# Kernel optimization log

Measured on AMD Instinct MI355X. Metric: run time of the kernel, lower is better.

## Reference

```python
import jax, jax.numpy as jnp
import numpy as np

B, N, K, IN_C, OUT_C = 8, 20000, 9, 64, 64


def setup_inputs() -> dict:
    key = jax.random.key(0)
    k1, k2, k3, k4, k5, k6 = jax.random.split(key, 6)
    x = jax.random.normal(k1, (B, N, IN_C), dtype=jnp.float32)
    neighbor_index = jax.random.randint(k2, (B, N, K), 0, N, dtype=jnp.int64)
    # adjweight initialized to identity per original code (eye expanded over num_pts)
    adjweight = jnp.broadcast_to(jnp.eye(K, dtype=jnp.float32), (N, K, K))
    # conv: Linear(in_c*K -> out_c); mlp_out: Linear(in_c -> out_c)
    conv_w = jax.random.normal(k3, (OUT_C, IN_C * K), dtype=jnp.float32) / np.sqrt(IN_C * K)
    conv_b = jax.random.normal(k4, (OUT_C,), dtype=jnp.float32) * 0.01
    mlp_w = jax.random.normal(k5, (OUT_C, IN_C), dtype=jnp.float32) / np.sqrt(IN_C)
    mlp_b = jax.random.normal(k6, (OUT_C,), dtype=jnp.float32) * 0.01
    return {"x": x, "neighbor_index": neighbor_index, "adjweight": adjweight,
            "conv_w": conv_w, "conv_b": conv_b, "mlp_w": mlp_w, "mlp_b": mlp_b}


def reference(x, neighbor_index, adjweight, conv_w, conv_b, mlp_w, mlp_b):
    bsize, num_pts, feats = x.shape
    num_neighbor = neighbor_index.shape[-1]
    # zero_padding mask: last point zeroed
    mask = jnp.ones((1, num_pts, 1), dtype=x.dtype).at[0, -1, 0].set(0.0)
    x = x * mask
    # per-batch gather of neighbor features: [B, N, K, F]
    x_neighbors = jax.vmap(lambda xb, ib: xb[ib])(x, neighbor_index)
    # learnable per-point KxK mixing over the neighbor dim: bnkf,nkt->bntf
    x_neighbors = jnp.einsum('bnkf,nkt->bntf', x_neighbors, adjweight)
    x_neighbors = jax.nn.elu(x_neighbors).reshape(bsize, num_pts, num_neighbor * feats)
    out_feat = jax.nn.elu(x_neighbors @ conv_w.T + conv_b) * mask
    x_res = x @ mlp_w.T + mlp_b
    return out_feat + x_res
```

## Files before the change

### kernel.cpp

```cpp
#include <hip/hip_runtime.h>

#define BB 8
#define NN 20000
#define KK 9
#define KC 576
#define ROWS (BB*NN)

#define WST_ELE   36864
#define WST2_ELE  4096
#define ADJ_ELE   (NN*88)
#define XB_ELE    (ROWS*64)
#define WST_OFF   0
#define WST2_OFF  36864
#define ADJ_OFF   40960
#define XB_OFF    (ADJ_OFF + ADJ_ELE)

typedef __bf16 bf16x8 __attribute__((ext_vector_type(8)));
typedef float  f32x4  __attribute__((ext_vector_type(4)));
typedef unsigned short u16x8 __attribute__((ext_vector_type(8)));
typedef unsigned u32x4 __attribute__((ext_vector_type(4)));

__device__ __forceinline__ unsigned short f2bf(float f) {
    unsigned u = __builtin_bit_cast(unsigned, f);
    u += 0x7FFFu + ((u >> 16) & 1u);
    return (unsigned short)(u >> 16);
}
__device__ __forceinline__ float bfhi2f(unsigned w) { return __builtin_bit_cast(float, w & 0xFFFF0000u); }
__device__ __forceinline__ float bflo2f(unsigned w) { return __builtin_bit_cast(float, w << 16); }
__device__ __forceinline__ float elu_f(float v) { return v > 0.0f ? v : (__expf(v) - 1.0f); }

__global__ void __launch_bounds__(256) paiconv_prep(
        const float* __restrict__ x,
        const float* __restrict__ adj,
        const float* __restrict__ conv_w,
        const float* __restrict__ mlp_w,
        unsigned short* __restrict__ ws16) {
    const int tid = blockIdx.x * 256 + threadIdx.x;

    if (tid < XB_ELE / 8) {
        const int e = tid * 8;
        const int r = e >> 6;
        const int n = r % NN;
        u16x8 pk;
        if (n == NN - 1) {
            #pragma unroll
            for (int i = 0; i < 8; ++i) pk[i] = 0;
        } else {
            f32x4 lo = *(const f32x4*)(x + e);
            f32x4 hi = *(const f32x4*)(x + e + 4);
            #pragma unroll
            for (int i = 0; i < 4; ++i) { pk[i] = f2bf(lo[i]); pk[4 + i] = f2bf(hi[i]); }
        }
        *(u16x8*)(ws16 + XB_OFF + e) = pk;
    }
    if (tid < NN * 11) {
        const int n = tid / 11;
        const int j = (tid - n * 11) * 8;
        u16x8 pk;
        #pragma unroll
        for (int m = 0; m < 8; ++m) {
            const int jj = j + m;
            pk[m] = (jj < 81) ? f2bf(adj[n * 81 + jj]) : (unsigned short)0;
        }
        *(u16x8*)(ws16 + ADJ_OFF + n * 88 + j) = pk;
    }
    if (tid < WST_ELE) {
        const int kk = tid & 31, o = (tid >> 5) & 63, mch = tid >> 11;
        const int c = mch / 9, t = mch - 9 * c;
        ws16[WST_OFF + tid] = f2bf(conv_w[o * KC + t * 64 + c * 32 + kk]);
    }
    if (tid < WST2_ELE) {
        const int kk = tid & 31, o = (tid >> 5) & 63, c2 = tid >> 11;
        ws16[WST2_OFF + tid] = f2bf(mlp_w[o * 64 + c2 * 32 + kk]);
    }
}

__global__ void __launch_bounds__(256, 2) paiconv_main(
        const int*   __restrict__ nidx,
        const float* __restrict__ conv_b,
        const float* __restrict__ mlp_b,
        const unsigned short* __restrict__ ws16,
        float* __restrict__ out) {
    __shared__ float sm[4][16][68];

    const int tx   = threadIdx.x;
    const int lane = tx & 63;
    const int l15  = lane & 15;
    const int q    = lane >> 4;
    const int wave = tx >> 6;
    const int batch = blockIdx.x & 7;
    const int chunk = blockIdx.x >> 3;
    const int n0    = chunk * 64 + wave * 16;
    if (n0 >= NN) return;
    const int rowbase = batch * NN + n0;
    const int myrow   = rowbase + l15;
    const int myn     = n0 + l15;

    const unsigned short* Wst  = ws16 + WST_OFF;
    const unsigned short* Wst2 = ws16 + WST2_OFF;
    const unsigned short* Adj  = ws16 + ADJ_OFF;
    const unsigned short* XB   = ws16 + XB_OFF;
    const unsigned short* XBb  = XB + (size_t)batch * NN * 64;

    int voff[KK];
    #pragma unroll
    for (int k = 0; k < KK; ++k) {
        const int idx = __builtin_nontemporal_load(nidx + myrow * KK + k);
        voff[k] = idx * 64 + q * 8;
    }

    unsigned adjw[44];
    {
        const u32x4* ap = (const u32x4*)(Adj + (size_t)myn * 88);
        #pragma unroll
        for (int u = 0; u < 11; ++u) {
            u32x4 w = __builtin_nontemporal_load(ap + u);
            adjw[4 * u + 0] = w.x; adjw[4 * u + 1] = w.y;
            adjw[4 * u + 2] = w.z; adjw[4 * u + 3] = w.w;
        }
    }

    f32x4 acc[4];
    f32x4 acc2[4];
    #pragma unroll
    for (int ot = 0; ot < 4; ++ot) { acc[ot] = (f32x4)0.0f; acc2[ot] = (f32x4)0.0f; }

    #pragma unroll 1
    for (int c = 0; c < 2; ++c) {
        float v[KK][8];
        #pragma unroll
        for (int k = 0; k < KK; ++k) {
            u16x8 pv = *(const u16x8*)(XBb + voff[k] + c * 32);
            u32x4 pw = __builtin_bit_cast(u32x4, pv);
            v[k][0] = bflo2f(pw.x); v[k][1] = bfhi2f(pw.x);
            v[k][2] = bflo2f(pw.y); v[k][3] = bfhi2f(pw.y);
            v[k][4] = bflo2f(pw.z); v[k][5] = bfhi2f(pw.z);
            v[k][6] = bflo2f(pw.w); v[k][7] = bfhi2f(pw.w);
        }
        #pragma unroll
        for (int t = 0; t < KK; ++t) {
            float m[8] = {0.f,0.f,0.f,0.f,0.f,0.f,0.f,0.f};
            #pragma unroll
            for (int k = 0; k < KK; ++k) {
                const int j = k * 9 + t;
                unsigned w = adjw[j >> 1];
                float a = (j & 1) ? bfhi2f(w) : bflo2f(w);
                #pragma unroll
                for (int i = 0; i < 8; ++i) m[i] = __builtin_fmaf(a, v[k][i], m[i]);
            }
            u16x8 pk;
            #pragma unroll
            for (int i = 0; i < 8; ++i) pk[i] = f2bf(elu_f(m[i]));
            bf16x8 afrag = __builtin_bit_cast(bf16x8, pk);
            const int mch = c * 9 + t;
            #pragma unroll
            for (int ot = 0; ot < 4; ++ot) {
                const u16x8* wp = (const u16x8*)(Wst + mch * 2048 + (ot * 16 + l15) * 32 + q * 8);
                bf16x8 bfrag = __builtin_bit_cast(bf16x8, *wp);
                acc[ot] = __builtin_amdgcn_mfma_f32_16x16x32_bf16(afrag, bfrag, acc[ot], 0, 0, 0);
            }
        }
    }

    #pragma unroll
    for (int c2 = 0; c2 < 2; ++c2) {
        bf16x8 a2 = *(const bf16x8*)(XB + (size_t)myrow * 64 + c2 * 32 + q * 8);
        #pragma unroll
        for (int ot = 0; ot < 4; ++ot) {
            const u16x8* wp = (const u16x8*)(Wst2 + c2 * 2048 + (ot * 16 + l15) * 32 + q * 8);
            bf16x8 b2 = __builtin_bit_cast(bf16x8, *wp);
            acc2[ot] = __builtin_amdgcn_mfma_f32_16x16x32_bf16(a2, b2, acc2[ot], 0, 0, 0);
        }
    }

    #pragma unroll
    for (int ot = 0; ot < 4; ++ot) {
        const int o = ot * 16 + l15;
        const float cb = conv_b[o];
        const float mb = mlp_b[o];
        #pragma unroll
        for (int i = 0; i < 4; ++i) {
            const int rr = 4 * q + i;
            float f = elu_f(acc[ot][i] + cb);
            if (n0 + rr == NN - 1) f = 0.0f;
            f += acc2[ot][i] + mb;
            sm[wave][rr][o] = f;
        }
    }
    #pragma unroll
    for (int p = 0; p < 4; ++p) {
        const int r = p * 4 + q;
        f32x4 vv = *(const f32x4*)&sm[wave][r][l15 * 4];
        __builtin_nontemporal_store(vv, (f32x4*)(out + (size_t)(rowbase + r) * 64 + l15 * 4));
    }
}

extern "C" void kernel_launch(void* const* d_in, const int* in_sizes, int n_in,
                              void* d_out, int out_size, void* d_ws, size_t ws_size,
                              hipStream_t stream) {
    const float* x      = (const float*)d_in[0];
    const int*   nidx   = (const int*)  d_in[1];
    const float* adj    = (const float*)d_in[2];
    const float* conv_w = (const float*)d_in[3];
    const float* conv_b = (const float*)d_in[4];
    const float* mlp_w  = (const float*)d_in[5];
    const float* mlp_b  = (const float*)d_in[6];
    unsigned short* ws16 = (unsigned short*)d_ws;
    float* out = (float*)d_out;

    const int prep_blocks = (XB_ELE / 8) / 256;
    paiconv_prep<<<prep_blocks, 256, 0, stream>>>(x, adj, conv_w, mlp_w, ws16);

    const int main_blocks = 8 * 313;
    paiconv_main<<<main_blocks, 256, 0, stream>>>(nidx, conv_b, mlp_b, ws16, out);
}
```

Baseline: 302.8 us.

## Restructure neighbor gather per-row across lanes and stage mixed features in LDS

The neighbor mixing is reorganised so that each wave processes one point at a time. The lanes span the 64 feature channels, the neighbor indices become wave-uniform scalar loads, and the adjacency weights are read straight from fp32 global memory instead of a bf16 copy made in the prep kernel. The mixed, ELU-activated features are written to an LDS tile, from which the MFMA A-fragments are then loaded. Blocks shrink to 128 threads with twice as many blocks. The intent is to drop the adjacency prep pass and the heavy per-lane register state, in exchange for serialised per-row gather latency, 16 sequential rows per wave, and extra LDS traffic.

```diff
diff --git a/kernel.cpp b/kernel.cpp
--- a/kernel.cpp
+++ b/kernel.cpp
@@ -8,30 +8,29 @@
 
 #define WST_ELE   36864
 #define WST2_ELE  4096
-#define ADJ_ELE   (NN*88)
 #define XB_ELE    (ROWS*64)
 #define WST_OFF   0
 #define WST2_OFF  36864
-#define ADJ_OFF   40960
-#define XB_OFF    (ADJ_OFF + ADJ_ELE)
+#define XB_OFF    40960
+
+#define PSTRIDE 584
 
 typedef __bf16 bf16x8 __attribute__((ext_vector_type(8)));
 typedef float  f32x4  __attribute__((ext_vector_type(4)));
 typedef unsigned short u16x8 __attribute__((ext_vector_type(8)));
-typedef unsigned u32x4 __attribute__((ext_vector_type(4)));
 
 __device__ __forceinline__ unsigned short f2bf(float f) {
     unsigned u = __builtin_bit_cast(unsigned, f);
     u += 0x7FFFu + ((u >> 16) & 1u);
     return (unsigned short)(u >> 16);
 }
-__device__ __forceinline__ float bfhi2f(unsigned w) { return __builtin_bit_cast(float, w & 0xFFFF0000u); }
-__device__ __forceinline__ float bflo2f(unsigned w) { return __builtin_bit_cast(float, w << 16); }
+__device__ __forceinline__ float bf2f(unsigned short h) {
+    return __builtin_bit_cast(float, ((unsigned)h) << 16);
+}
 __device__ __forceinline__ float elu_f(float v) { return v > 0.0f ? v : (__expf(v) - 1.0f); }
 
 __global__ void __launch_bounds__(256) paiconv_prep(
         const float* __restrict__ x,
-        const float* __restrict__ adj,
         const float* __restrict__ conv_w,
         const float* __restrict__ mlp_w,
         unsigned short* __restrict__ ws16) {
@@ -53,17 +52,6 @@
         }
         *(u16x8*)(ws16 + XB_OFF + e) = pk;
     }
-    if (tid < NN * 11) {
-        const int n = tid / 11;
-        const int j = (tid - n * 11) * 8;
-        u16x8 pk;
-        #pragma unroll
-        for (int m = 0; m < 8; ++m) {
-            const int jj = j + m;
-            pk[m] = (jj < 81) ? f2bf(adj[n * 81 + jj]) : (unsigned short)0;
-        }
-        *(u16x8*)(ws16 + ADJ_OFF + n * 88 + j) = pk;
-    }
     if (tid < WST_ELE) {
         const int kk = tid & 31, o = (tid >> 5) & 63, mch = tid >> 11;
         const int c = mch / 9, t = mch - 9 * c;
@@ -75,49 +63,54 @@
     }
 }
 
-__global__ void __launch_bounds__(256, 2) paiconv_main(
+__global__ void __launch_bounds__(128, 2) paiconv_main(
         const int*   __restrict__ nidx,
+        const float* __restrict__ adj,
         const float* __restrict__ conv_b,
         const float* __restrict__ mlp_b,
         const unsigned short* __restrict__ ws16,
         float* __restrict__ out) {
-    __shared__ float sm[4][16][68];
+    __shared__ unsigned short P[2][16 * PSTRIDE];
 
     const int tx   = threadIdx.x;
     const int lane = tx & 63;
     const int l15  = lane & 15;
     const int q    = lane >> 4;
-    const int wave = tx >> 6;
+    const int wave = __builtin_amdgcn_readfirstlane(tx >> 6);
     const int batch = blockIdx.x & 7;
     const int chunk = blockIdx.x >> 3;
-    const int n0    = chunk * 64 + wave * 16;
-    if (n0 >= NN) return;
+    const int n0    = chunk * 32 + wave * 16;
     const int rowbase = batch * NN + n0;
-    const int myrow   = rowbase + l15;
-    const int myn     = n0 + l15;
 
     const unsigned short* Wst  = ws16 + WST_OFF;
     const unsigned short* Wst2 = ws16 + WST2_OFF;
-    const unsigned short* Adj  = ws16 + ADJ_OFF;
     const unsigned short* XB   = ws16 + XB_OFF;
     const unsigned short* XBb  = XB + (size_t)batch * NN * 64;
+    unsigned short* Pw = &P[wave][0];
 
-    int voff[KK];
-    #pragma unroll
-    for (int k = 0; k < KK; ++k) {
-        const int idx = __builtin_nontemporal_load(nidx + myrow * KK + k);
-        voff[k] = idx * 64 + q * 8;
-    }
+    #pragma unroll 2
+    for (int r = 0; r < 16; ++r) {
+        const int n    = n0 + r;
+        const int grow = rowbase + r;
+        const float* adjrow = adj + (size_t)n * 81;
 
-    unsigned adjw[44];
-    {
-        const u32x4* ap = (const u32x4*)(Adj + (size_t)myn * 88);
+        float vf[KK];
         #pragma unroll
-        for (int u = 0; u < 11; ++u) {
-            u32x4 w = __builtin_nontemporal_load(ap + u);
-            adjw[4 * u + 0] = w.x; adjw[4 * u + 1] = w.y;
-            adjw[4 * u + 2] = w.z; adjw[4 * u + 3] = w.w;
+        for (int k = 0; k < KK; ++k) {
+            const int idx = __builtin_amdgcn_readfirstlane(nidx[grow * KK + k]);
+            const unsigned short* rp = XBb + idx * 64;
+            vf[k] = bf2f(rp[lane]);
         }
+        float m[KK] = {0.f,0.f,0.f,0.f,0.f,0.f,0.f,0.f,0.f};
+        #pragma unroll
+        for (int k = 0; k < KK; ++k) {
+            #pragma unroll
+            for (int t = 0; t < KK; ++t)
+                m[t] = __builtin_fmaf(adjrow[k * 9 + t], vf[k], m[t]);
+        }
+        #pragma unroll
+        for (int t = 0; t < KK; ++t)
+            Pw[r * PSTRIDE + t * 64 + lane] = f2bf(elu_f(m[t]));
     }
 
     f32x4 acc[4];
@@ -125,33 +118,12 @@
     #pragma unroll
     for (int ot = 0; ot < 4; ++ot) { acc[ot] = (f32x4)0.0f; acc2[ot] = (f32x4)0.0f; }
 
-    #pragma unroll 1
+    #pragma unroll
     for (int c = 0; c < 2; ++c) {
-        float v[KK][8];
-        #pragma unroll
-        for (int k = 0; k < KK; ++k) {
-            u16x8 pv = *(const u16x8*)(XBb + voff[k] + c * 32);
-            u32x4 pw = __builtin_bit_cast(u32x4, pv);
-            v[k][0] = bflo2f(pw.x); v[k][1] = bfhi2f(pw.x);
-            v[k][2] = bflo2f(pw.y); v[k][3] = bfhi2f(pw.y);
-            v[k][4] = bflo2f(pw.z); v[k][5] = bfhi2f(pw.z);
-            v[k][6] = bflo2f(pw.w); v[k][7] = bfhi2f(pw.w);
-        }
         #pragma unroll
         for (int t = 0; t < KK; ++t) {
-            float m[8] = {0.f,0.f,0.f,0.f,0.f,0.f,0.f,0.f};
-            #pragma unroll
-            for (int k = 0; k < KK; ++k) {
-                const int j = k * 9 + t;
-                unsigned w = adjw[j >> 1];
-                float a = (j & 1) ? bfhi2f(w) : bflo2f(w);
-                #pragma unroll
-                for (int i = 0; i < 8; ++i) m[i] = __builtin_fmaf(a, v[k][i], m[i]);
-            }
-            u16x8 pk;
-            #pragma unroll
-            for (int i = 0; i < 8; ++i) pk[i] = f2bf(elu_f(m[i]));
-            bf16x8 afrag = __builtin_bit_cast(bf16x8, pk);
+            const u16x8* ap = (const u16x8*)(Pw + l15 * PSTRIDE + t * 64 + c * 32 + q * 8);
+            bf16x8 afrag = __builtin_bit_cast(bf16x8, *ap);
             const int mch = c * 9 + t;
             #pragma unroll
             for (int ot = 0; ot < 4; ++ot) {
@@ -164,7 +136,7 @@
 
     #pragma unroll
     for (int c2 = 0; c2 < 2; ++c2) {
-        bf16x8 a2 = *(const bf16x8*)(XB + (size_t)myrow * 64 + c2 * 32 + q * 8);
+        bf16x8 a2 = *(const bf16x8*)(XB + (size_t)(rowbase + l15) * 64 + c2 * 32 + q * 8);
         #pragma unroll
         for (int ot = 0; ot < 4; ++ot) {
             const u16x8* wp = (const u16x8*)(Wst2 + c2 * 2048 + (ot * 16 + l15) * 32 + q * 8);
@@ -173,6 +145,7 @@
         }
     }
 
+    float* smf = (float*)Pw;
     #pragma unroll
     for (int ot = 0; ot < 4; ++ot) {
         const int o = ot * 16 + l15;
@@ -184,14 +157,14 @@
             float f = elu_f(acc[ot][i] + cb);
             if (n0 + rr == NN - 1) f = 0.0f;
             f += acc2[ot][i] + mb;
-            sm[wave][rr][o] = f;
+            smf[rr * 68 + o] = f;
         }
     }
     #pragma unroll
     for (int p = 0; p < 4; ++p) {
         const int r = p * 4 + q;
-        f32x4 vv = *(const f32x4*)&sm[wave][r][l15 * 4];
-        __builtin_nontemporal_store(vv, (f32x4*)(out + (size_t)(rowbase + r) * 64 + l15 * 4));
+        f32x4 vv = *(const f32x4*)&smf[r * 68 + l15 * 4];
+        *(f32x4*)(out + (size_t)(rowbase + r) * 64 + l15 * 4) = vv;
     }
 }
 
@@ -209,8 +182,8 @@
     float* out = (float*)d_out;
 
     const int prep_blocks = (XB_ELE / 8) / 256;
-    paiconv_prep<<<prep_blocks, 256, 0, stream>>>(x, adj, conv_w, mlp_w, ws16);
+    paiconv_prep<<<prep_blocks, 256, 0, stream>>>(x, conv_w, mlp_w, ws16);
 
-    const int main_blocks = 8 * 313;
-    paiconv_main<<<main_blocks, 256, 0, stream>>>(nidx, conv_b, mlp_b, ws16, out);
+    const int main_blocks = 8 * 625;
+    paiconv_main<<<main_blocks, 128, 0, stream>>>(nidx, adj, conv_b, mlp_b, ws16, out);
 }
```

Result: faster. 252.7 us (-16.5%).
